# Kernel tuning notes

Hardware: AMD Instinct MI355X
Metric: run time of the kernel (lower is better)

## Reference

```python
import jax, jax.numpy as jnp
import numpy as np

N_NODES = 1_000_000
N_EDGES = 16_000_000
NUM_REL = 3
C_IN, C_OUT = 3, 2


def setup_inputs() -> dict:
    key = jax.random.key(0)
    ks = jax.random.split(key, 10)
    x = jax.random.normal(ks[0], (N_NODES, C_IN), dtype=jnp.float32)
    edge_index = jax.random.randint(ks[1], (2, N_EDGES), 0, N_NODES, dtype=jnp.int64)
    edge_attr = jax.random.randint(ks[2], (N_EDGES,), 0, NUM_REL, dtype=jnp.int64)
    s = 0.3
    W1 = jax.random.normal(ks[3], (NUM_REL, C_IN, C_OUT), dtype=jnp.float32) * s
    root1 = jax.random.normal(ks[4], (C_IN, C_OUT), dtype=jnp.float32) * s
    b1 = jax.random.normal(ks[5], (C_OUT,), dtype=jnp.float32) * s
    W2 = jax.random.normal(ks[6], (NUM_REL, C_OUT, C_OUT), dtype=jnp.float32) * s
    root2 = jax.random.normal(ks[7], (C_OUT, C_OUT), dtype=jnp.float32) * s
    b2 = jax.random.normal(ks[8], (C_OUT,), dtype=jnp.float32) * s
    return {"x": x, "edge_index": edge_index, "edge_attr": edge_attr,
            "W1": W1, "root1": root1, "b1": b1,
            "W2": W2, "root2": root2, "b2": b2}


def rgcn_conv(x, edge_index, edge_type, W, root, bias, num_nodes):
    """PyG RGCNConv: per-relation mean-aggregated messages + root transform + bias."""
    src, dst = edge_index[0], edge_index[1]
    xs = x[src]                                    # [E, c_in] gather once
    out = x @ root + bias                          # [N, c_out]
    for r in range(NUM_REL):                       # small fixed relation loop
        mask = (edge_type == r)
        msg = jnp.where(mask[:, None], xs @ W[r], 0.0)          # [E, c_out]
        sums = jax.ops.segment_sum(msg, dst, num_segments=num_nodes)
        cnt = jax.ops.segment_sum(mask.astype(x.dtype), dst, num_segments=num_nodes)
        out = out + sums / jnp.maximum(cnt, 1.0)[:, None]       # mean aggr
    return out


def reference(x, edge_index, edge_attr, W1, root1, b1, W2, root2, b2):
    h = rgcn_conv(x, edge_index, edge_attr, W1, root1, b1, N_NODES)
    h = jax.nn.relu(h)
    # F.dropout(training=self.training): identity in eval mode
    out = rgcn_conv(h, edge_index, edge_attr, W2, root2, b2, N_NODES)
    return out
```

## Files before the change

### kernel.cpp

```cpp
#include <hip/hip_runtime.h>


typedef unsigned long long u64;
typedef unsigned u32;

constexpr int NN = 1000000;
constexpr int NE = 16000000;
constexpr int NR = 3;

constexpr int BSH   = 10;
constexpr int NB    = (NN + 1023) >> 10;
constexpr int BCAP  = 18432;
constexpr int EPB   = 16384;
constexpr int NBLKB = (NE + EPB - 1) / EPB;

constexpr u64 M28 = (1ULL << 28) - 1;

__device__ __forceinline__ u64 pack_msg(float m0, float m1) {
    int a0 = __float2int_rn(fmaf(m0, 4096.0f, 524288.0f));
    int a1 = __float2int_rn(fmaf(m1, 4096.0f, 524288.0f));
    return (u64)(u32)a0 | ((u64)(u32)a1 << 28) | (1ULL << 56);
}

__device__ __forceinline__ u32 enc_x(float x0, float x1, float x2) {
    int q0 = __float2int_rn(fminf(fmaxf(x0 * 64.0f, -511.0f), 511.0f));
    int q1 = __float2int_rn(fminf(fmaxf(x1 * 128.0f, -1023.0f), 1023.0f));
    int q2 = __float2int_rn(fminf(fmaxf(x2 * 128.0f, -1023.0f), 1023.0f));
    return ((u32)q0 & 0x3FFu) | (((u32)q1 & 0x7FFu) << 10) | (((u32)q2 & 0x7FFu) << 21);
}

__device__ __forceinline__ void dec_x(u32 e, float& x0, float& x1, float& x2) {
    x0 = (float)((int)(e << 22) >> 22) * (1.0f / 64.0f);
    x1 = (float)((int)(e << 11) >> 21) * (1.0f / 128.0f);
    x2 = (float)((int)e >> 21)         * (1.0f / 128.0f);
}

__device__ __forceinline__ u32 enc_h(float h0, float h1) {
    int q0 = __float2int_rn(fminf(h0 * 1024.0f, 32767.0f));
    int q1 = __float2int_rn(fminf(h1 * 1024.0f, 32767.0f));
    return ((u32)q0 & 0xFFFFu) | ((u32)q1 << 16);
}

__device__ __forceinline__ void dec_h(u32 e, float& h0, float& h1) {
    h0 = (float)((int)(e << 16) >> 16) * (1.0f / 1024.0f);
    h1 = (float)((int)e >> 16)         * (1.0f / 1024.0f);
}


__global__ __launch_bounds__(256) void prep_qx_kernel(
    const float* __restrict__ x, u32* __restrict__ qx)
{
    int n = blockIdx.x * 256 + threadIdx.x;
    if (n >= NN) return;
    qx[n] = enc_x(x[3 * n + 0], x[3 * n + 1], x[3 * n + 2]);
}

__global__ __launch_bounds__(1024) void scatter_kernel(
    const int* __restrict__ src, const int* __restrict__ dst, const int* __restrict__ rel,
    u32* __restrict__ buf, u32* __restrict__ cursor)
{
    __shared__ u32 stage[EPB];
    __shared__ u32 hist[1024];
    __shared__ u32 wcur[1024];
    __shared__ u32 gbase[1024];
    __shared__ u32 wt[16];
    const int tid = threadIdx.x;
    const int wave = tid >> 6, lane = tid & 63;

    hist[tid] = 0;
    __syncthreads();

    const int base = blockIdx.x * EPB;
    const int nloc = min(EPB, NE - base);

    for (int i = tid; i < nloc; i += 1024)
        atomicAdd(&hist[((u32)dst[base + i]) >> BSH], 1u);
    __syncthreads();

    {
        int h0 = hist[tid];
        int v0 = h0;
#pragma unroll
        for (int d = 1; d < 64; d <<= 1) {
            int t = __shfl_up(v0, d);
            if (lane >= d) v0 += t;
        }
        if (lane == 63) wt[wave] = (u32)v0;
        __syncthreads();
        u32 off = 0;
#pragma unroll
        for (int wv = 0; wv < 16; ++wv) off += (wv < wave) ? wt[wv] : 0u;
        wcur[tid] = off + (u32)(v0 - h0);
    }
    __syncthreads();

    if (tid < NB) {
        u32 c = hist[tid];
        gbase[tid] = c ? atomicAdd(&cursor[tid], c) : 0u;
    }
    __syncthreads();

    for (int i = tid; i < nloc; i += 1024) {
        int e = base + i;
        u32 d = (u32)dst[e];
        u32 bk = d >> BSH;
        u32 sl = atomicAdd(&wcur[bk], 1u);
        stage[sl] = (u32)src[e] | ((u32)rel[e] << 20) | ((d & 1023u) << 22);
    }
    __syncthreads();

    for (int b = wave; b < NB; b += 16) {
        u32 cnt = hist[b];
        if (!cnt) continue;
        u32 ls = wcur[b] - cnt;
        u32 gb = gbase[b];
        u32* bb = buf + (size_t)b * BCAP;
        for (u32 j = lane; j < cnt; j += 64) {
            u32 slot = gb + j;
            if (slot < (u32)BCAP) bb[slot] = stage[ls + j];
        }
    }
}

__global__ __launch_bounds__(512) void agg1_kernel(
    const u32* __restrict__ buf, const u32* __restrict__ cursor,
    const u32* __restrict__ qx, const float* __restrict__ x,
    const float* __restrict__ W1,
    const float* __restrict__ root1, const float* __restrict__ b1,
    u32* __restrict__ qh)
{
    __shared__ u64 acc[1024 * NR];
    __shared__ float w[NR * 3 * 2];
    const int tid = threadIdx.x;
    for (int i = tid; i < 1024 * NR; i += 512) acc[i] = 0;
    if (tid < NR * 3 * 2) w[tid] = W1[tid];
    __syncthreads();

    const int bk = blockIdx.x;
    const int n = min((int)cursor[bk], BCAP);
    const u32* bb = buf + (size_t)bk * BCAP;

    int i = tid;
    for (; i + 3584 < n; i += 4096) {
        u32 e[8], g[8];
#pragma unroll
        for (int j = 0; j < 8; ++j) e[j] = bb[i + 512 * j];
#pragma unroll
        for (int j = 0; j < 8; ++j) g[j] = qx[e[j] & 0xFFFFFu];
#pragma unroll
        for (int j = 0; j < 8; ++j) {
            float a, b, c;
            dec_x(g[j], a, b, c);
            u32 r = (e[j] >> 20) & 3u; const float* wr = &w[r * 6];
            atomicAdd(&acc[(e[j] >> 22) * NR + r],
                pack_msg(a * wr[0] + b * wr[2] + c * wr[4],
                         a * wr[1] + b * wr[3] + c * wr[5]));
        }
    }
    for (; i < n; i += 512) {
        u32 e0 = bb[i];
        u32 g0 = qx[e0 & 0xFFFFFu];
        float a, b, c;
        dec_x(g0, a, b, c);
        u32 r = (e0 >> 20) & 3u; const float* wr = &w[r * 6];
        atomicAdd(&acc[(e0 >> 22) * NR + r],
            pack_msg(a * wr[0] + b * wr[2] + c * wr[4],
                     a * wr[1] + b * wr[3] + c * wr[5]));
    }
    __syncthreads();

    for (int l = tid; l < 1024; l += 512) {
        int node = (bk << BSH) + l;
        if (node >= NN) continue;
        float x0 = x[3 * node + 0], x1 = x[3 * node + 1], x2 = x[3 * node + 2];
        float o0 = x0 * root1[0] + x1 * root1[2] + x2 * root1[4] + b1[0];
        float o1 = x0 * root1[1] + x1 * root1[3] + x2 * root1[5] + b1[1];
#pragma unroll
        for (int r = 0; r < NR; ++r) {
            u64 wv = acc[l * NR + r];
            int c = (int)(wv >> 56);
            int s0i = (int)(wv & M28) - (c << 19);
            int s1i = (int)((wv >> 28) & M28) - (c << 19);
            float inv = (1.0f / 4096.0f) / (float)(c > 1 ? c : 1);
            o0 += (float)s0i * inv;
            o1 += (float)s1i * inv;
        }
        qh[node] = enc_h(fmaxf(o0, 0.0f), fmaxf(o1, 0.0f));
    }
}

__global__ __launch_bounds__(512) void agg2_kernel(
    const u32* __restrict__ buf, const u32* __restrict__ cursor,
    const u32* __restrict__ qh, const float* __restrict__ W2,
    const float* __restrict__ root2, const float* __restrict__ b2,
    float* __restrict__ out)
{
    __shared__ u64 acc[1024 * NR];
    __shared__ float w[NR * 2 * 2];
    const int tid = threadIdx.x;
    for (int i = tid; i < 1024 * NR; i += 512) acc[i] = 0;
    if (tid < NR * 2 * 2) w[tid] = W2[tid];
    __syncthreads();

    const int bk = blockIdx.x;
    const int n = min((int)cursor[bk], BCAP);
    const u32* bb = buf + (size_t)bk * BCAP;

    int i = tid;
    for (; i + 3584 < n; i += 4096) {
        u32 e[8], g[8];
#pragma unroll
        for (int j = 0; j < 8; ++j) e[j] = bb[i + 512 * j];
#pragma unroll
        for (int j = 0; j < 8; ++j) g[j] = qh[e[j] & 0xFFFFFu];
#pragma unroll
        for (int j = 0; j < 8; ++j) {
            float a, b;
            dec_h(g[j], a, b);
            u32 r = (e[j] >> 20) & 3u; const float* wr = &w[r * 4];
            atomicAdd(&acc[(e[j] >> 22) * NR + r],
                pack_msg(a * wr[0] + b * wr[2], a * wr[1] + b * wr[3]));
        }
    }
    for (; i < n; i += 512) {
        u32 e0 = bb[i];
        u32 g0 = qh[e0 & 0xFFFFFu];
        float a, b;
        dec_h(g0, a, b);
        u32 r = (e0 >> 20) & 3u; const float* wr = &w[r * 4];
        atomicAdd(&acc[(e0 >> 22) * NR + r],
            pack_msg(a * wr[0] + b * wr[2], a * wr[1] + b * wr[3]));
    }
    __syncthreads();

    for (int l = tid; l < 1024; l += 512) {
        int node = (bk << BSH) + l;
        if (node >= NN) continue;
        float hv0, hv1;
        dec_h(qh[node], hv0, hv1);
        float o0 = hv0 * root2[0] + hv1 * root2[2] + b2[0];
        float o1 = hv0 * root2[1] + hv1 * root2[3] + b2[1];
#pragma unroll
        for (int r = 0; r < NR; ++r) {
            u64 wv = acc[l * NR + r];
            int c = (int)(wv >> 56);
            int s0i = (int)(wv & M28) - (c << 19);
            int s1i = (int)((wv >> 28) & M28) - (c << 19);
            float inv = (1.0f / 4096.0f) / (float)(c > 1 ? c : 1);
            o0 += (float)s0i * inv;
            o1 += (float)s1i * inv;
        }
        float2 ov; ov.x = o0; ov.y = o1;
        ((float2*)out)[node] = ov;
    }
}


__global__ __launch_bounds__(256) void edge1_kernel(
    const int* __restrict__ src, const int* __restrict__ dst, const int* __restrict__ rel,
    const float* __restrict__ x, const float* __restrict__ W1,
    u64* __restrict__ sums1)
{
    __shared__ float w[NR * 3 * 2];
    if (threadIdx.x < NR * 3 * 2) w[threadIdx.x] = W1[threadIdx.x];
    __syncthreads();
    int e = blockIdx.x * 256 + threadIdx.x;
    if (e >= NE) return;
    int s = src[e], d = dst[e], r = rel[e];
    float x0 = x[3 * s + 0], x1 = x[3 * s + 1], x2 = x[3 * s + 2];
    const float* wr = &w[r * 6];
    float m0 = x0 * wr[0] + x1 * wr[2] + x2 * wr[4];
    float m1 = x0 * wr[1] + x1 * wr[3] + x2 * wr[5];
    atomicAdd(&sums1[d * NR + r], pack_msg(m0, m1));
}

__global__ __launch_bounds__(256) void node1_kernel(
    const float* __restrict__ x, const u64* __restrict__ sums1,
    const float* __restrict__ root1, const float* __restrict__ b1,
    float* __restrict__ h)
{
    int n = blockIdx.x * 256 + threadIdx.x;
    if (n >= NN) return;
    float x0 = x[3 * n + 0], x1 = x[3 * n + 1], x2 = x[3 * n + 2];
    float o0 = x0 * root1[0] + x1 * root1[2] + x2 * root1[4] + b1[0];
    float o1 = x0 * root1[1] + x1 * root1[3] + x2 * root1[5] + b1[1];
#pragma unroll
    for (int r = 0; r < NR; ++r) {
        u64 wv = sums1[n * NR + r];
        int c = (int)(wv >> 56);
        int s0i = (int)(wv & M28) - (c << 19);
        int s1i = (int)((wv >> 28) & M28) - (c << 19);
        float inv = (1.0f / 4096.0f) / (float)(c > 1 ? c : 1);
        o0 += (float)s0i * inv;
        o1 += (float)s1i * inv;
    }
    float2 hv;
    hv.x = fmaxf(o0, 0.0f);
    hv.y = fmaxf(o1, 0.0f);
    ((float2*)h)[n] = hv;
}

__global__ __launch_bounds__(256) void edge2_kernel(
    const int* __restrict__ src, const int* __restrict__ dst, const int* __restrict__ rel,
    const float* __restrict__ h, const float* __restrict__ W2,
    u64* __restrict__ sums2)
{
    __shared__ float w[NR * 2 * 2];
    if (threadIdx.x < NR * 2 * 2) w[threadIdx.x] = W2[threadIdx.x];
    __syncthreads();
    int e = blockIdx.x * 256 + threadIdx.x;
    if (e >= NE) return;
    int s = src[e];
    float2 hs = ((const float2*)h)[s];
    if (hs.x == 0.0f && hs.y == 0.0f) return;
    int d = dst[e], r = rel[e];
    const float* wr = &w[r * 4];
    float m0 = hs.x * wr[0] + hs.y * wr[2];
    float m1 = hs.x * wr[1] + hs.y * wr[3];
    atomicAdd(&sums2[d * NR + r], pack_msg(m0, m1));
}

__global__ __launch_bounds__(256) void node2_kernel(
    const float* __restrict__ h, const u64* __restrict__ sums1, const u64* __restrict__ sums2,
    const float* __restrict__ root2, const float* __restrict__ b2,
    float* __restrict__ out)
{
    int n = blockIdx.x * 256 + threadIdx.x;
    if (n >= NN) return;
    float2 hv = ((const float2*)h)[n];
    float o0 = hv.x * root2[0] + hv.y * root2[2] + b2[0];
    float o1 = hv.x * root2[1] + hv.y * root2[3] + b2[1];
#pragma unroll
    for (int r = 0; r < NR; ++r) {
        u64 w1 = sums1[n * NR + r];
        u64 w2 = sums2[n * NR + r];
        int c    = (int)(w1 >> 56);
        int adds = (int)(w2 >> 56);
        int s0i = (int)(w2 & M28) - (adds << 19);
        int s1i = (int)((w2 >> 28) & M28) - (adds << 19);
        float inv = (1.0f / 4096.0f) / (float)(c > 1 ? c : 1);
        o0 += (float)s0i * inv;
        o1 += (float)s1i * inv;
    }
    float2 ov; ov.x = o0; ov.y = o1;
    ((float2*)out)[n] = ov;
}

extern "C" void kernel_launch(void* const* d_in, const int* in_sizes, int n_in,
                              void* d_out, int out_size, void* d_ws, size_t ws_size,
                              hipStream_t stream) {
    const float* x     = (const float*)d_in[0];
    const int*   ei    = (const int*)d_in[1];
    const int*   rel   = (const int*)d_in[2];
    const float* W1    = (const float*)d_in[3];
    const float* root1 = (const float*)d_in[4];
    const float* b1    = (const float*)d_in[5];
    const float* W2    = (const float*)d_in[6];
    const float* root2 = (const float*)d_in[7];
    const float* b2    = (const float*)d_in[8];
    float* out = (float*)d_out;

    const int* src = ei;
    const int* dst = ei + NE;

    char* ws = (char*)d_ws;
    const int nb = (NN + 255) / 256;

    const size_t OFF_QX  = 72024064;
    const size_t OFF_QH  = 76024064;
    const size_t OFF_CUR = 80024064;
    const size_t WS_NEED = OFF_CUR + (size_t)NB * sizeof(u32);

    if (ws_size >= WS_NEED) {
        u32* buf    = (u32*)ws;
        u32* qx     = (u32*)(ws + OFF_QX);
        u32* qh     = (u32*)(ws + OFF_QH);
        u32* cursor = (u32*)(ws + OFF_CUR);

        hipMemsetAsync(cursor, 0, (size_t)NB * sizeof(u32), stream);
        prep_qx_kernel<<<nb, 256, 0, stream>>>(x, qx);
        scatter_kernel<<<NBLKB, 1024, 0, stream>>>(src, dst, rel, buf, cursor);
        agg1_kernel<<<NB, 512, 0, stream>>>(buf, cursor, qx, x, W1, root1, b1, qh);
        agg2_kernel<<<NB, 512, 0, stream>>>(buf, cursor, qh, W2, root2, b2, out);
    } else {
        u64*   sums1 = (u64*)ws;
        u64*   sums2 = (u64*)(ws + (size_t)24 * 1000 * 1000);
        float* h     = (float*)(ws + (size_t)48 * 1000 * 1000);
        const int eb = (NE + 255) / 256;

        hipMemsetAsync(sums1, 0, (size_t)NN * NR * sizeof(u64), stream);
        hipMemsetAsync(sums2, 0, (size_t)NN * NR * sizeof(u64), stream);
        edge1_kernel<<<eb, 256, 0, stream>>>(src, dst, rel, x, W1, sums1);
        node1_kernel<<<nb, 256, 0, stream>>>(x, sums1, root1, b1, h);
        edge2_kernel<<<eb, 256, 0, stream>>>(src, dst, rel, h, W2, sums2);
        node2_kernel<<<nb, 256, 0, stream>>>(h, sums1, sums2, root2, b2, out);
    }
}
```

Before: 483.5 us.

## Fuse qx prep into scatter, cache edges in registers, use nontemporal memory ops

The scatter kernel now reads each edge's src, dst and rel once into registers during the histogram pass and reuses them for staging, instead of reading global memory twice. The separate qx quantization kernel is folded into the scatter kernel, which removes one launch. Streamed edge-buffer loads and stores and the final output stores become nontemporal to reduce cache pollution. In exchange, the 16-entry per-thread register arrays raise register pressure in the 1024-thread scatter blocks. Fusing qx assumes the 977 scatter blocks cover all nodes, and since NBLKB is 977 they do.

```diff
diff --git a/kernel.cpp b/kernel.cpp
--- a/kernel.cpp
+++ b/kernel.cpp
@@ -3,6 +3,7 @@
 
 typedef unsigned long long u64;
 typedef unsigned u32;
+typedef float vfloat2 __attribute__((ext_vector_type(2)));
 
 constexpr int NN = 1000000;
 constexpr int NE = 16000000;
@@ -13,6 +14,7 @@
 constexpr int BCAP  = 18432;
 constexpr int EPB   = 16384;
 constexpr int NBLKB = (NE + EPB - 1) / EPB;
+constexpr int EPT   = EPB / 1024;
 
 constexpr u64 M28 = (1ULL << 28) - 1;
 
@@ -47,16 +49,9 @@
 }
 
 
-__global__ __launch_bounds__(256) void prep_qx_kernel(
-    const float* __restrict__ x, u32* __restrict__ qx)
-{
-    int n = blockIdx.x * 256 + threadIdx.x;
-    if (n >= NN) return;
-    qx[n] = enc_x(x[3 * n + 0], x[3 * n + 1], x[3 * n + 2]);
-}
-
-__global__ __launch_bounds__(1024) void scatter_kernel(
+__global__ __launch_bounds__(1024, 8) void scatter_kernel(
     const int* __restrict__ src, const int* __restrict__ dst, const int* __restrict__ rel,
+    const float* __restrict__ x, u32* __restrict__ qx,
     u32* __restrict__ buf, u32* __restrict__ cursor)
 {
     __shared__ u32 stage[EPB];
@@ -73,8 +68,20 @@
     const int base = blockIdx.x * EPB;
     const int nloc = min(EPB, NE - base);
 
-    for (int i = tid; i < nloc; i += 1024)
-        atomicAdd(&hist[((u32)dst[base + i]) >> BSH], 1u);
+    u32 rent[EPT], rbk[EPT];
+#pragma unroll
+    for (int k = 0; k < EPT; ++k) {
+        int i = tid + (k << 10);
+        if (i < nloc) {
+            int e = base + i;
+            u32 d = (u32)__builtin_nontemporal_load(&dst[e]);
+            u32 s = (u32)__builtin_nontemporal_load(&src[e]);
+            u32 r = (u32)__builtin_nontemporal_load(&rel[e]);
+            rbk[k]  = d >> BSH;
+            rent[k] = s | (r << 20) | ((d & 1023u) << 22);
+            atomicAdd(&hist[rbk[k]], 1u);
+        }
+    }
     __syncthreads();
 
     {
@@ -98,14 +105,21 @@
         u32 c = hist[tid];
         gbase[tid] = c ? atomicAdd(&cursor[tid], c) : 0u;
     }
-    __syncthreads();
-
-    for (int i = tid; i < nloc; i += 1024) {
-        int e = base + i;
-        u32 d = (u32)dst[e];
-        u32 bk = d >> BSH;
-        u32 sl = atomicAdd(&wcur[bk], 1u);
-        stage[sl] = (u32)src[e] | ((u32)rel[e] << 20) | ((d & 1023u) << 22);
+
+    {
+        int node = (blockIdx.x << BSH) + tid;
+        if (node < NN)
+            qx[node] = enc_x(x[3 * node + 0], x[3 * node + 1], x[3 * node + 2]);
+    }
+    __syncthreads();
+
+#pragma unroll
+    for (int k = 0; k < EPT; ++k) {
+        int i = tid + (k << 10);
+        if (i < nloc) {
+            u32 sl = atomicAdd(&wcur[rbk[k]], 1u);
+            stage[sl] = rent[k];
+        }
     }
     __syncthreads();
 
@@ -117,7 +131,8 @@
         u32* bb = buf + (size_t)b * BCAP;
         for (u32 j = lane; j < cnt; j += 64) {
             u32 slot = gb + j;
-            if (slot < (u32)BCAP) bb[slot] = stage[ls + j];
+            if (slot < (u32)BCAP)
+                __builtin_nontemporal_store(stage[ls + j], &bb[slot]);
         }
     }
 }
@@ -144,7 +159,7 @@
     for (; i + 3584 < n; i += 4096) {
         u32 e[8], g[8];
 #pragma unroll
-        for (int j = 0; j < 8; ++j) e[j] = bb[i + 512 * j];
+        for (int j = 0; j < 8; ++j) e[j] = __builtin_nontemporal_load(&bb[i + 512 * j]);
 #pragma unroll
         for (int j = 0; j < 8; ++j) g[j] = qx[e[j] & 0xFFFFFu];
 #pragma unroll
@@ -158,7 +173,7 @@
         }
     }
     for (; i < n; i += 512) {
-        u32 e0 = bb[i];
+        u32 e0 = __builtin_nontemporal_load(&bb[i]);
         u32 g0 = qx[e0 & 0xFFFFFu];
         float a, b, c;
         dec_x(g0, a, b, c);
@@ -210,7 +225,7 @@
     for (; i + 3584 < n; i += 4096) {
         u32 e[8], g[8];
 #pragma unroll
-        for (int j = 0; j < 8; ++j) e[j] = bb[i + 512 * j];
+        for (int j = 0; j < 8; ++j) e[j] = __builtin_nontemporal_load(&bb[i + 512 * j]);
 #pragma unroll
         for (int j = 0; j < 8; ++j) g[j] = qh[e[j] & 0xFFFFFu];
 #pragma unroll
@@ -223,7 +238,7 @@
         }
     }
     for (; i < n; i += 512) {
-        u32 e0 = bb[i];
+        u32 e0 = __builtin_nontemporal_load(&bb[i]);
         u32 g0 = qh[e0 & 0xFFFFFu];
         float a, b;
         dec_h(g0, a, b);
@@ -250,8 +265,9 @@
             o0 += (float)s0i * inv;
             o1 += (float)s1i * inv;
         }
-        float2 ov; ov.x = o0; ov.y = o1;
-        ((float2*)out)[node] = ov;
+        vfloat2 ov;
+        ov.x = o0; ov.y = o1;
+        __builtin_nontemporal_store(ov, (vfloat2*)((float2*)out + node));
     }
 }
 
@@ -364,7 +380,6 @@
     const int* dst = ei + NE;
 
     char* ws = (char*)d_ws;
-    const int nb = (NN + 255) / 256;
 
     const size_t OFF_QX  = 72024064;
     const size_t OFF_QH  = 76024064;
@@ -378,8 +393,7 @@
         u32* cursor = (u32*)(ws + OFF_CUR);
 
         hipMemsetAsync(cursor, 0, (size_t)NB * sizeof(u32), stream);
-        prep_qx_kernel<<<nb, 256, 0, stream>>>(x, qx);
-        scatter_kernel<<<NBLKB, 1024, 0, stream>>>(src, dst, rel, buf, cursor);
+        scatter_kernel<<<NBLKB, 1024, 0, stream>>>(src, dst, rel, x, qx, buf, cursor);
         agg1_kernel<<<NB, 512, 0, stream>>>(buf, cursor, qx, x, W1, root1, b1, qh);
         agg2_kernel<<<NB, 512, 0, stream>>>(buf, cursor, qh, W2, root2, b2, out);
     } else {
@@ -387,6 +401,7 @@
         u64*   sums2 = (u64*)(ws + (size_t)24 * 1000 * 1000);
         float* h     = (float*)(ws + (size_t)48 * 1000 * 1000);
         const int eb = (NE + 255) / 256;
+        const int nb = (NN + 255) / 256;
 
         hipMemsetAsync(sums1, 0, (size_t)NN * NR * sizeof(u64), stream);
         hipMemsetAsync(sums2, 0, (size_t)NN * NR * sizeof(u64), stream);
```

Measured after the change: 503.4 us. 1.04x slower.
